# Kernel tuning notes

Hardware: AMD Instinct MI355X
Metric: run time of the kernel (lower is better)

The kernel has to match this reference:

```python
import jax, jax.numpy as jnp
import numpy as np

TAU = 10.0
AMP_FACTOR = 6.0
BLOCK = 10  # each pixel -> 8x8 value block padded by 1 -> 10x10


def _make_h(size=200, wavelength=5.32e-07, pixel_size=3.6e-05, distance=0.1):
    ll = pixel_size * size
    fi = 1.0 / ll
    wn = 2 * 3.1415926 / wavelength
    phi = np.fromfunction(
        lambda x, y: np.square((x - size // 2) * fi) + np.square((y - size // 2) * fi),
        shape=(size, size), dtype=np.float64)
    h = np.fft.fftshift(np.exp(1j * wn * distance) * np.exp(-1j * wavelength * np.pi * distance * phi))
    return h.astype(np.complex64)


def setup_inputs() -> dict:
    key = jax.random.key(0)
    B, S, P = 16, 200, 256
    ks = jax.random.split(key, 5)
    h = _make_h(size=S)
    return {
        "waves_real": jax.random.normal(ks[0], (B, S, S), jnp.float32),
        "waves_imag": jax.random.normal(ks[1], (B, S, S), jnp.float32),
        "h_real": jnp.asarray(h.real, jnp.float32),
        "h_imag": jnp.asarray(h.imag, jnp.float32),
        "voltage": jax.random.uniform(ks[2], (S, S, P), jnp.float32),
        "phase_func": jax.random.uniform(ks[3], (P,), jnp.float32),
        "intensity_func": jax.random.uniform(ks[4], (P,), jnp.float32),
    }


def _gumbel_softmax_hard(logits, key, tau):
    u = jax.random.uniform(key, logits.shape, logits.dtype, 1e-10, 1.0)
    g = -jnp.log(-jnp.log(u))
    y_soft = jax.nn.softmax((logits + g) / tau, axis=-1)
    y_hard = jax.nn.one_hot(jnp.argmax(y_soft, axis=-1), logits.shape[-1], dtype=logits.dtype)
    # straight-through estimator
    return y_hard + y_soft - jax.lax.stop_gradient(y_soft)


def reference(waves_real, waves_imag, h_real, h_imag, voltage, phase_func, intensity_func):
    waves = waves_real + 1j * waves_imag              # (B,S,S) complex
    h = h_real + 1j * h_imag                          # (S,S) complex transfer fn
    temp = jnp.fft.ifft2(jnp.fft.fft2(waves) * h)     # free-space diffraction

    k1, k2 = jax.random.split(jax.random.key(42))
    exp_j_phase = _gumbel_softmax_hard(voltage, k1, TAU) @ phase_func      # (S,S)
    amplitude = (_gumbel_softmax_hard(voltage, k2, TAU) @ intensity_func) * AMP_FACTOR
    phase_trig = amplitude * (jnp.cos(exp_j_phase) + 1j * jnp.sin(exp_j_phase))
    x = temp * phase_trig                             # (B,S,S) complex

    # pixel expansion: each pixel -> 10x10 block (value in center 8x8, zero border)
    B, S = x.shape[0], x.shape[1]
    pat = jnp.zeros((BLOCK, BLOCK), x.dtype).at[1:9, 1:9].set(1.0)
    out = (x[:, :, None, :, None] * pat[None, :, None, :][None]).reshape(B, S * BLOCK, S * BLOCK)
    return jnp.stack([out.real, out.imag], axis=-1)   # (B, 10S, 10S, 2) float
```

## Files before the change

kernel.cpp:

```cpp
#include <hip/hip_runtime.h>
#include <math.h>

constexpr int S = 200;
constexpr int NBATCH = 16;
constexpr int SS = S * S;
constexpr int FLAT = S * NBATCH;
constexpr int SLICE = S * FLAT;

struct TFOut { unsigned a, b; };

__host__ __device__ constexpr TFOut tf2x32(unsigned k0, unsigned k1,
                                           unsigned x0, unsigned x1) {
  unsigned ks2 = k0 ^ k1 ^ 0x1BD11BDAu;
  unsigned ks[3] = {k0, k1, ks2};
  const int R0[4] = {13, 15, 26, 6};
  const int R1[4] = {17, 29, 16, 24};
  x0 += ks[0]; x1 += ks[1];
  for (int i = 0; i < 5; ++i) {
    const int* R = (i & 1) ? R1 : R0;
    for (int j = 0; j < 4; ++j) {
      x0 += x1;
      x1 = (x1 << R[j]) | (x1 >> (32 - R[j]));
      x1 ^= x0;
    }
    x0 += ks[(i + 1) % 3];
    x1 += ks[(i + 2) % 3] + (unsigned)(i + 1);
  }
  return {x0, x1};
}

constexpr TFOut KEY1 = tf2x32(0u, 42u, 0u, 0u);
constexpr TFOut KEY2 = tf2x32(0u, 42u, 0u, 1u);

__device__ inline float bits_to_u(unsigned bits) {
  float f = __uint_as_float((bits >> 9) | 0x3f800000u) - 1.0f;
  f = f + 1e-10f;
  return fmaxf(1e-10f, f);
}

__device__ inline float u_to_g_exact(float u) {
  float l1 = (float)log((double)u);
  float l2 = (float)log((double)(-l1));
  return -l2;
}

__device__ inline float u_to_g_fast(float u) {
  float l1 = logf(u);
  float l2 = logf(-l1);
  return -l2;
}

__device__ inline unsigned ordf(float f) {
  unsigned u = __float_as_uint(f);
  return (u & 0x80000000u) ? ~u : (u | 0x80000000u);
}
__device__ inline float unordf(unsigned u) {
  return (u & 0x80000000u) ? __uint_as_float(u ^ 0x80000000u)
                           : __uint_as_float(~u);
}
__device__ inline unsigned long long packcand(float val, int p) {
  return ((unsigned long long)ordf(val) << 32) | (unsigned)(255 - p);
}
__device__ inline unsigned long long umax64(unsigned long long a,
                                            unsigned long long b) {
  return a > b ? a : b;
}
__device__ inline unsigned long long wave_max_ull(unsigned long long v) {
#pragma unroll
  for (int s = 32; s > 0; s >>= 1)
    v = umax64(v, (unsigned long long)__shfl_xor((unsigned long long)v, s, 64));
  return v;
}

__global__ __launch_bounds__(256) void gumbel_kernel(
    const float* __restrict__ voltage, const float* __restrict__ phase_func,
    const float* __restrict__ intensity_func, float2* __restrict__ PT) {
  const int q = blockIdx.x;
  const int p = threadIdx.x;
  const int wave = p >> 6, lane = p & 63;
  const unsigned idx = (unsigned)q * 256u + (unsigned)p;
  const float v = voltage[(size_t)q * 256 + p];
  TFOut r1 = tf2x32(KEY1.a, KEY1.b, 0u, idx);
  TFOut r2 = tf2x32(KEY2.a, KEY2.b, 0u, idx);
  const float u1 = bits_to_u(r1.a ^ r1.b);
  const float u2 = bits_to_u(r2.a ^ r2.b);
  const float c1a = (v + u_to_g_fast(u1)) * 0.1f;
  const float c2a = (v + u_to_g_fast(u2)) * 0.1f;

  __shared__ unsigned long long wred[2][4];
  __shared__ int wcnt[2][4];

  unsigned long long pk1 = wave_max_ull(packcand(c1a, p));
  unsigned long long pk2 = wave_max_ull(packcand(c2a, p));
  if (lane == 0) { wred[0][wave] = pk1; wred[1][wave] = pk2; }
  __syncthreads();
  unsigned long long b1 = umax64(umax64(wred[0][0], wred[0][1]),
                                 umax64(wred[0][2], wred[0][3]));
  unsigned long long b2 = umax64(umax64(wred[1][0], wred[1][1]),
                                 umax64(wred[1][2], wred[1][3]));
  const float eps = 1e-5f;
  const bool q1 = c1a >= unordf((unsigned)(b1 >> 32)) - eps;
  const bool q2 = c2a >= unordf((unsigned)(b2 >> 32)) - eps;
  unsigned long long bal1 = __ballot(q1);
  unsigned long long bal2 = __ballot(q2);
  if (lane == 0) { wcnt[0][wave] = __popcll(bal1); wcnt[1][wave] = __popcll(bal2); }
  __syncthreads();
  const int n1 = wcnt[0][0] + wcnt[0][1] + wcnt[0][2] + wcnt[0][3];
  const int n2 = wcnt[1][0] + wcnt[1][1] + wcnt[1][2] + wcnt[1][3];

  unsigned long long w1 = b1, w2 = b2;
  if (n1 > 1 || n2 > 1) {
    unsigned long long e1 = q1 ? packcand((v + u_to_g_exact(u1)) / 10.0f, p) : 0ull;
    unsigned long long e2 = q2 ? packcand((v + u_to_g_exact(u2)) / 10.0f, p) : 0ull;
    e1 = wave_max_ull(e1);
    e2 = wave_max_ull(e2);
    if (lane == 0) { wred[0][wave] = e1; wred[1][wave] = e2; }
    __syncthreads();
    w1 = umax64(umax64(wred[0][0], wred[0][1]), umax64(wred[0][2], wred[0][3]));
    w2 = umax64(umax64(wred[1][0], wred[1][1]), umax64(wred[1][2], wred[1][3]));
  }
  if (p == 0) {
    int i1 = 255 - (int)(w1 & 0xFFFFFFFFull);
    int i2 = 255 - (int)(w2 & 0xFFFFFFFFull);
    float phi = phase_func[i1];
    float amp = intensity_func[i2] * 6.0f;
    PT[q] = make_float2(amp * cosf(phi), amp * sinf(phi));
  }
}

__global__ __launch_bounds__(256) void build_tw(float2* __restrict__ tw) {
  int m = threadIdx.x;
  if (m < S) {
    double ang = -2.0 * 3.1415926535897932384626433832795 * (double)m / (double)S;
    tw[m] = make_float2((float)cos(ang), (float)sin(ang));
  }
}

__global__ __launch_bounds__(256) void build_tables(
    const float* __restrict__ h_real, const float* __restrict__ h_imag,
    const float2* __restrict__ tw, float2* __restrict__ F,
    float2* __restrict__ G, float2* __restrict__ Hc) {
  int idx = blockIdx.x * 256 + threadIdx.x;
  if (idx >= SS) return;
  int j = idx / S;
  int k = idx - j * S;
  int m = (j * k) % S;
  float2 t = tw[m];
  F[idx] = t;
  G[idx] = make_float2(t.x * 0.005f, -t.y * 0.005f);
  Hc[idx] = make_float2(h_real[idx], h_imag[idx]);
}

template <bool APERM, int MODE>
__global__ __launch_bounds__(256) void cgemm_ks(
    const float2* __restrict__ A, const float2* __restrict__ B,
    const float* __restrict__ Bre, const float* __restrict__ Bim,
    const float2* __restrict__ Hm, float2* __restrict__ Cp,
    int M, int N, int K, int KSlice) {
  __shared__ __align__(16) float2 As[16][64];
  __shared__ __align__(16) float2 Bs[16][64];
  const int tid = threadIdx.x;
  const int rowBase = blockIdx.x * 64;
  const int colBase = blockIdx.y * 64;
  const int Kbeg = blockIdx.z * KSlice;
  const int Kend = min(Kbeg + KSlice, K);

  const int a_m = tid >> 2;
  const int a_k4 = (tid & 3) * 4;
  const int b_k = tid >> 4;
  const int b_n4 = (tid & 15) * 4;
  const int tx4 = (tid & 15) * 4;
  const int ty4 = (tid >> 4) * 4;

  long arow;
  bool arow_ok;
  {
    int gm = rowBase + a_m;
    if (APERM) {
      int b = gm / S, i = gm - b * S;
      arow = (long)i * FLAT + (long)b * S;
      arow_ok = true;
    } else {
      arow_ok = (gm < M);
      arow = (long)gm * S;
    }
  }
  long bcol;
  int nmod = 0;
  bool bcol_ok;
  {
    int gn = colBase + b_n4;
    if (APERM) {
      bcol = gn;
      bcol_ok = (gn < N);
    } else {
      int b = gn / S;
      nmod = gn - b * S;
      bcol = (long)b * SS + nmod;
      bcol_ok = true;
    }
  }

  float2 acc[4][4];
#pragma unroll
  for (int i = 0; i < 4; ++i)
#pragma unroll
    for (int j = 0; j < 4; ++j) acc[i][j] = make_float2(0.f, 0.f);

  for (int k0 = Kbeg; k0 < Kend; k0 += 16) {
    const int gka = k0 + a_k4;
    float4 av0 = {0, 0, 0, 0}, av1 = {0, 0, 0, 0};
    if (arow_ok) {
      if (gka < Kend) av0 = *(const float4*)&A[arow + gka];
      if (gka + 2 < Kend) av1 = *(const float4*)&A[arow + gka + 2];
    }
    const int gkb = k0 + b_k;
    float4 bv0 = {0, 0, 0, 0}, bv1 = {0, 0, 0, 0};
    if (bcol_ok && gkb < Kend) {
      if (MODE == 2) {
        const long off = bcol + (long)gkb * S;
        float4 re4 = *(const float4*)&Bre[off];
        float4 im4 = *(const float4*)&Bim[off];
        bv0 = make_float4(re4.x, im4.x, re4.y, im4.y);
        bv1 = make_float4(re4.z, im4.z, re4.w, im4.w);
      } else {
        const float2* bp = &B[bcol + (long)gkb * S];
        bv0 = *(const float4*)bp;
        bv1 = *(const float4*)(bp + 2);
        if (MODE == 1) {
          const float2* hp = &Hm[(long)gkb * S + nmod];
          float4 h0 = *(const float4*)hp;
          float4 h1 = *(const float4*)(hp + 2);
          bv0 = make_float4(bv0.x * h0.x - bv0.y * h0.y, bv0.x * h0.y + bv0.y * h0.x,
                            bv0.z * h0.z - bv0.w * h0.w, bv0.z * h0.w + bv0.w * h0.z);
          bv1 = make_float4(bv1.x * h1.x - bv1.y * h1.y, bv1.x * h1.y + bv1.y * h1.x,
                            bv1.z * h1.z - bv1.w * h1.w, bv1.z * h1.w + bv1.w * h1.z);
        }
      }
    }
    __syncthreads();
    As[a_k4 + 0][a_m] = make_float2(av0.x, av0.y);
    As[a_k4 + 1][a_m] = make_float2(av0.z, av0.w);
    As[a_k4 + 2][a_m] = make_float2(av1.x, av1.y);
    As[a_k4 + 3][a_m] = make_float2(av1.z, av1.w);
    *(float4*)&Bs[b_k][b_n4] = bv0;
    *(float4*)&Bs[b_k][b_n4 + 2] = bv1;
    __syncthreads();
#pragma unroll
    for (int kk = 0; kk < 16; ++kk) {
      float4 aA = *(const float4*)&As[kk][ty4];
      float4 aB = *(const float4*)&As[kk][ty4 + 2];
      float4 bA = *(const float4*)&Bs[kk][tx4];
      float4 bB = *(const float4*)&Bs[kk][tx4 + 2];
      float2 a[4] = {{aA.x, aA.y}, {aA.z, aA.w}, {aB.x, aB.y}, {aB.z, aB.w}};
      float2 b[4] = {{bA.x, bA.y}, {bA.z, bA.w}, {bB.x, bB.y}, {bB.z, bB.w}};
#pragma unroll
      for (int i = 0; i < 4; ++i)
#pragma unroll
        for (int j = 0; j < 4; ++j) {
          acc[i][j].x = fmaf(a[i].x, b[j].x, fmaf(-a[i].y, b[j].y, acc[i][j].x));
          acc[i][j].y = fmaf(a[i].x, b[j].y, fmaf(a[i].y, b[j].x, acc[i][j].y));
        }
    }
  }
  float2* Co = Cp + (long)blockIdx.z * SLICE;
#pragma unroll
  for (int rr = 0; rr < 4; ++rr) {
    const int r = rowBase + ty4 + rr;
    const int cb = colBase + tx4;
    if (r < M && cb < N) {
      *(float4*)&Co[(long)r * N + cb] = make_float4(acc[rr][0].x, acc[rr][0].y,
                                                    acc[rr][1].x, acc[rr][1].y);
      *(float4*)&Co[(long)r * N + cb + 2] = make_float4(acc[rr][2].x, acc[rr][2].y,
                                                        acc[rr][3].x, acc[rr][3].y);
    }
  }
}

__global__ __launch_bounds__(256) void reduce4(
    const float4* __restrict__ P, float4* __restrict__ D) {
  int i = blockIdx.x * 256 + threadIdx.x;
  if (i >= SLICE / 2) return;
  float4 a = P[i], b = P[i + SLICE / 2], c = P[i + SLICE], d = P[i + 3 * SLICE / 2];
  D[i] = make_float4(a.x + b.x + c.x + d.x, a.y + b.y + c.y + d.y,
                     a.z + b.z + c.z + d.z, a.w + b.w + c.w + d.w);
}

__global__ __launch_bounds__(256) void reduce4_pt(
    const float2* __restrict__ P, const float2* __restrict__ PT,
    float2* __restrict__ D) {
  int i = blockIdx.x * 256 + threadIdx.x;
  if (i >= SLICE) return;
  float2 a = P[i], b = P[i + SLICE], c = P[i + 2 * SLICE], d = P[i + 3 * SLICE];
  float sx = a.x + b.x + c.x + d.x;
  float sy = a.y + b.y + c.y + d.y;
  float2 pt = PT[i % SS];
  D[i] = make_float2(sx * pt.x - sy * pt.y, sx * pt.y + sy * pt.x);
}

__global__ __launch_bounds__(256) void expand_kernel(
    const float2* __restrict__ Xc, float4* __restrict__ out) {
  unsigned q = blockIdx.x * 256u + threadIdx.x;
  unsigned p0 = q * 2u;
  unsigned b = p0 / 4000000u;
  unsigned rem = p0 - b * 4000000u;
  unsigned r = rem / 2000u;
  unsigned c0 = rem - r * 2000u;
  unsigned i = r / 10u;
  unsigned dr = r - i * 10u;
  float4 o = {0.f, 0.f, 0.f, 0.f};
  if (dr - 1u <= 7u) {
    unsigned j = c0 / 10u;
    unsigned dc = c0 - j * 10u;
    float2 xv = Xc[b * 40000u + i * 200u + j];
    if (dc != 0u) { o.x = xv.x; o.y = xv.y; }
    if (dc != 8u) { o.z = xv.x; o.w = xv.y; }
  }
  out[q] = o;
}

extern "C" void kernel_launch(void* const* d_in, const int* in_sizes, int n_in,
                              void* d_out, int out_size, void* d_ws, size_t ws_size,
                              hipStream_t stream) {
  const float* waves_real = (const float*)d_in[0];
  const float* waves_imag = (const float*)d_in[1];
  const float* h_real = (const float*)d_in[2];
  const float* h_imag = (const float*)d_in[3];
  const float* voltage = (const float*)d_in[4];
  const float* phase_func = (const float*)d_in[5];
  const float* intensity_func = (const float*)d_in[6];

  float2* TW   = (float2*)d_ws;
  float2* F    = TW + 256;
  float2* G    = F + SS;
  float2* Hc   = G + SS;
  float2* PT   = Hc + SS;
  float2* T1   = PT + SS;
  float2* T2   = T1 + SLICE;
  float2* T4   = T2 + SLICE;
  float2* Xc   = T4 + SLICE;
  float2* Part = Xc + SLICE;

  build_tw<<<1, 256, 0, stream>>>(TW);
  build_tables<<<157, 256, 0, stream>>>(h_real, h_imag, TW, F, G, Hc);
  gumbel_kernel<<<40000, 256, 0, stream>>>(voltage, phase_func, intensity_func, PT);

  dim3 gB(4, 50, 4);
  dim3 gA(50, 4, 4);

  cgemm_ks<false, 2><<<gB, 256, 0, stream>>>(F, nullptr, waves_real, waves_imag,
                                             nullptr, Part, S, FLAT, S, 50);
  reduce4<<<1250, 256, 0, stream>>>((const float4*)Part, (float4*)T1);
  cgemm_ks<true, 0><<<gA, 256, 0, stream>>>(T1, F, nullptr, nullptr, nullptr,
                                            Part, FLAT, S, S, 50);
  reduce4<<<1250, 256, 0, stream>>>((const float4*)Part, (float4*)T2);
  cgemm_ks<false, 1><<<gB, 256, 0, stream>>>(G, T2, nullptr, nullptr, Hc,
                                             Part, S, FLAT, S, 50);
  reduce4<<<1250, 256, 0, stream>>>((const float4*)Part, (float4*)T4);
  cgemm_ks<true, 0><<<gA, 256, 0, stream>>>(T4, G, nullptr, nullptr, nullptr,
                                            Part, FLAT, S, S, 50);
  reduce4_pt<<<2500, 256, 0, stream>>>(Part, PT, Xc);

  expand_kernel<<<125000, 256, 0, stream>>>(Xc, (float4*)d_out);
}
```

Baseline: 740.0 us.

## Replace FP32 split-K complex GEMMs with split-bf16 MFMA GEMMs and transposed layouts

Replaces the four FP32 CUDA-core complex DFT GEMMs and their split-K partial sums plus reduction kernels with an MFMA bf16 GEMM. Each operand is split into high and low bf16 parts, and three MFMAs per product approximate fp32 accuracy. Intermediates are stored transposed so each stage reads the previous one along K, and the final phase multiply is fused into the last GEMM epilogue. This removes the reduction passes and their partial-sum traffic. The costs are extra bf16 split work in the B loads, uncoalesced strided B loads in mode 0, and a precision risk from the bf16x3 approximation.

```diff
diff --git a/kernel.cpp b/kernel.cpp
--- a/kernel.cpp
+++ b/kernel.cpp
@@ -2,10 +2,15 @@
 #include <math.h>
 
 constexpr int S = 200;
-constexpr int NBATCH = 16;
 constexpr int SS = S * S;
-constexpr int FLAT = S * NBATCH;
-constexpr int SLICE = S * FLAT;
+constexpr int FLAT = 3200;
+constexpr int SLICE = 640000;
+constexpr int MP = 256;
+constexpr int KP = 224;
+constexpr int PS = MP * KP;
+
+typedef short short8 __attribute__((ext_vector_type(8)));
+typedef float float4v __attribute__((ext_vector_type(4)));
 
 struct TFOut { unsigned a, b; };
 
@@ -37,19 +42,16 @@
   f = f + 1e-10f;
   return fmaxf(1e-10f, f);
 }
-
 __device__ inline float u_to_g_exact(float u) {
   float l1 = (float)log((double)u);
   float l2 = (float)log((double)(-l1));
   return -l2;
 }
-
 __device__ inline float u_to_g_fast(float u) {
   float l1 = logf(u);
   float l2 = logf(-l1);
   return -l2;
 }
-
 __device__ inline unsigned ordf(float f) {
   unsigned u = __float_as_uint(f);
   return (u & 0x80000000u) ? ~u : (u | 0x80000000u);
@@ -136,170 +138,193 @@
   }
 }
 
-__global__ __launch_bounds__(256) void build_tables(
+__device__ inline unsigned short bf16_rne(float x) {
+  unsigned u = __float_as_uint(x);
+  return (unsigned short)((u + 0x7FFFu + ((u >> 16) & 1u)) >> 16);
+}
+__device__ inline void split_bf16(float x, unsigned short& h, unsigned short& l) {
+  h = bf16_rne(x);
+  float hf = __uint_as_float(((unsigned)h) << 16);
+  l = bf16_rne(x - hf);
+}
+
+__global__ __launch_bounds__(256) void build_planes(
+    const float2* __restrict__ tw, unsigned short* __restrict__ PL) {
+  int idx = blockIdx.x * 256 + threadIdx.x;
+  int m = idx / KP, k = idx - (idx / KP) * KP;
+  float fr = 0.f, fi = 0.f;
+  if (m < S && k < S) {
+    float2 t = tw[(m * k) % S];
+    fr = t.x; fi = t.y;
+  }
+  unsigned short h, l;
+  split_bf16(fr, h, l);          PL[0 * PS + idx] = h; PL[1 * PS + idx] = l;
+  split_bf16(fi, h, l);          PL[2 * PS + idx] = h; PL[3 * PS + idx] = l;
+  split_bf16(fr * 0.005f, h, l); PL[4 * PS + idx] = h; PL[5 * PS + idx] = l;
+  split_bf16(-fi * 0.005f, h, l);PL[6 * PS + idx] = h; PL[7 * PS + idx] = l;
+}
+
+__global__ __launch_bounds__(256) void build_ht(
     const float* __restrict__ h_real, const float* __restrict__ h_imag,
-    const float2* __restrict__ tw, float2* __restrict__ F,
-    float2* __restrict__ G, float2* __restrict__ Hc) {
+    float2* __restrict__ HT) {
   int idx = blockIdx.x * 256 + threadIdx.x;
   if (idx >= SS) return;
-  int j = idx / S;
-  int k = idx - j * S;
-  int m = (j * k) % S;
-  float2 t = tw[m];
-  F[idx] = t;
-  G[idx] = make_float2(t.x * 0.005f, -t.y * 0.005f);
-  Hc[idx] = make_float2(h_real[idx], h_imag[idx]);
-}
-
-template <bool APERM, int MODE>
-__global__ __launch_bounds__(256) void cgemm_ks(
-    const float2* __restrict__ A, const float2* __restrict__ B,
-    const float* __restrict__ Bre, const float* __restrict__ Bim,
-    const float2* __restrict__ Hm, float2* __restrict__ Cp,
-    int M, int N, int K, int KSlice) {
-  __shared__ __align__(16) float2 As[16][64];
-  __shared__ __align__(16) float2 Bs[16][64];
+  int k = idx / S, n = idx - (idx / S) * S;
+  HT[n * S + k] = make_float2(h_real[idx], h_imag[idx]);
+}
+
+template <int MODE, bool FINAL>
+__global__ __launch_bounds__(256) void gemm_mfma(
+    const unsigned short* __restrict__ APL, const float* __restrict__ Wre,
+    const float* __restrict__ Wim, const float2* __restrict__ Sprev,
+    const float2* __restrict__ HT, const float2* __restrict__ PT,
+    float2* __restrict__ Sout) {
+  __shared__ short As[4][64][40];
+  __shared__ short Bs[4][64][40];
   const int tid = threadIdx.x;
-  const int rowBase = blockIdx.x * 64;
-  const int colBase = blockIdx.y * 64;
-  const int Kbeg = blockIdx.z * KSlice;
-  const int Kend = min(Kbeg + KSlice, K);
-
-  const int a_m = tid >> 2;
-  const int a_k4 = (tid & 3) * 4;
-  const int b_k = tid >> 4;
-  const int b_n4 = (tid & 15) * 4;
-  const int tx4 = (tid & 15) * 4;
-  const int ty4 = (tid >> 4) * 4;
-
-  long arow;
-  bool arow_ok;
-  {
-    int gm = rowBase + a_m;
-    if (APERM) {
-      int b = gm / S, i = gm - b * S;
-      arow = (long)i * FLAT + (long)b * S;
-      arow_ok = true;
-    } else {
-      arow_ok = (gm < M);
-      arow = (long)gm * S;
-    }
-  }
-  long bcol;
-  int nmod = 0;
-  bool bcol_ok;
-  {
-    int gn = colBase + b_n4;
-    if (APERM) {
-      bcol = gn;
-      bcol_ok = (gn < N);
-    } else {
-      int b = gn / S;
-      nmod = gn - b * S;
-      bcol = (long)b * SS + nmod;
-      bcol_ok = true;
-    }
-  }
-
-  float2 acc[4][4];
-#pragma unroll
-  for (int i = 0; i < 4; ++i)
-#pragma unroll
-    for (int j = 0; j < 4; ++j) acc[i][j] = make_float2(0.f, 0.f);
-
-  for (int k0 = Kbeg; k0 < Kend; k0 += 16) {
-    const int gka = k0 + a_k4;
-    float4 av0 = {0, 0, 0, 0}, av1 = {0, 0, 0, 0};
-    if (arow_ok) {
-      if (gka < Kend) av0 = *(const float4*)&A[arow + gka];
-      if (gka + 2 < Kend) av1 = *(const float4*)&A[arow + gka + 2];
-    }
-    const int gkb = k0 + b_k;
-    float4 bv0 = {0, 0, 0, 0}, bv1 = {0, 0, 0, 0};
-    if (bcol_ok && gkb < Kend) {
-      if (MODE == 2) {
-        const long off = bcol + (long)gkb * S;
-        float4 re4 = *(const float4*)&Bre[off];
-        float4 im4 = *(const float4*)&Bim[off];
-        bv0 = make_float4(re4.x, im4.x, re4.y, im4.y);
-        bv1 = make_float4(re4.z, im4.z, re4.w, im4.w);
+  const int wave = tid >> 6, lane = tid & 63, quad = lane >> 4, l15 = lane & 15;
+  const int mb = blockIdx.x * 64;
+  const int cb = blockIdx.y * 64;
+
+  const int sp = tid >> 6;
+  const int sm = tid & 63;
+  const int sn = tid & 63;
+  const int sk0 = (tid >> 6) * 8;
+  const int cB = cb + sn;
+  const int bB = cB / S;
+  const int nB = cB - bB * S;
+
+  float4v accRR[2][2], accII[2][2], accRI[2][2], accIR[2][2];
+#pragma unroll
+  for (int i = 0; i < 2; ++i)
+#pragma unroll
+    for (int j = 0; j < 2; ++j) {
+      accRR[i][j] = (float4v){0.f, 0.f, 0.f, 0.f};
+      accII[i][j] = (float4v){0.f, 0.f, 0.f, 0.f};
+      accRI[i][j] = (float4v){0.f, 0.f, 0.f, 0.f};
+      accIR[i][j] = (float4v){0.f, 0.f, 0.f, 0.f};
+    }
+
+  for (int ch = 0; ch < 7; ++ch) {
+    const int kc = ch * 32;
+    const unsigned short* ap = APL + sp * PS + (mb + sm) * KP + kc;
+    short8 a0 = *(const short8*)(ap + 0);
+    short8 a1 = *(const short8*)(ap + 8);
+    short8 a2 = *(const short8*)(ap + 16);
+    short8 a3 = *(const short8*)(ap + 24);
+
+    unsigned short brh[8], brl[8], bih[8], bil[8];
+    const bool kok = (kc + sk0) < S;
+    float re[8], im[8];
+#pragma unroll
+    for (int j = 0; j < 8; ++j) { re[j] = 0.f; im[j] = 0.f; }
+    if (kok) {
+      if (MODE == 0) {
+#pragma unroll
+        for (int j = 0; j < 8; ++j) {
+          int k = kc + sk0 + j;
+          re[j] = Wre[(long)bB * SS + k * S + nB];
+          im[j] = Wim[(long)bB * SS + k * S + nB];
+        }
       } else {
-        const float2* bp = &B[bcol + (long)gkb * S];
-        bv0 = *(const float4*)bp;
-        bv1 = *(const float4*)(bp + 2);
-        if (MODE == 1) {
-          const float2* hp = &Hm[(long)gkb * S + nmod];
-          float4 h0 = *(const float4*)hp;
-          float4 h1 = *(const float4*)(hp + 2);
-          bv0 = make_float4(bv0.x * h0.x - bv0.y * h0.y, bv0.x * h0.y + bv0.y * h0.x,
-                            bv0.z * h0.z - bv0.w * h0.w, bv0.z * h0.w + bv0.w * h0.z);
-          bv1 = make_float4(bv1.x * h1.x - bv1.y * h1.y, bv1.x * h1.y + bv1.y * h1.x,
-                            bv1.z * h1.z - bv1.w * h1.w, bv1.z * h1.w + bv1.w * h1.z);
+        const float2* bp = &Sprev[(long)(bB * S + nB) * S + kc + sk0];
+#pragma unroll
+        for (int j = 0; j < 8; ++j) { re[j] = bp[j].x; im[j] = bp[j].y; }
+        if (MODE == 2) {
+          const float2* hp = &HT[(long)nB * S + kc + sk0];
+#pragma unroll
+          for (int j = 0; j < 8; ++j) {
+            float2 hv = hp[j];
+            float tr = re[j] * hv.x - im[j] * hv.y;
+            im[j] = re[j] * hv.y + im[j] * hv.x;
+            re[j] = tr;
+          }
         }
       }
     }
+#pragma unroll
+    for (int j = 0; j < 8; ++j) {
+      split_bf16(re[j], brh[j], brl[j]);
+      split_bf16(im[j], bih[j], bil[j]);
+    }
+
     __syncthreads();
-    As[a_k4 + 0][a_m] = make_float2(av0.x, av0.y);
-    As[a_k4 + 1][a_m] = make_float2(av0.z, av0.w);
-    As[a_k4 + 2][a_m] = make_float2(av1.x, av1.y);
-    As[a_k4 + 3][a_m] = make_float2(av1.z, av1.w);
-    *(float4*)&Bs[b_k][b_n4] = bv0;
-    *(float4*)&Bs[b_k][b_n4 + 2] = bv1;
+    *(short8*)&As[sp][sm][0] = a0;
+    *(short8*)&As[sp][sm][8] = a1;
+    *(short8*)&As[sp][sm][16] = a2;
+    *(short8*)&As[sp][sm][24] = a3;
+    short8 v0, v1, v2, v3;
+#pragma unroll
+    for (int j = 0; j < 8; ++j) {
+      v0[j] = (short)brh[j]; v1[j] = (short)brl[j];
+      v2[j] = (short)bih[j]; v3[j] = (short)bil[j];
+    }
+    *(short8*)&Bs[0][sn][sk0] = v0;
+    *(short8*)&Bs[1][sn][sk0] = v1;
+    *(short8*)&Bs[2][sn][sk0] = v2;
+    *(short8*)&Bs[3][sn][sk0] = v3;
     __syncthreads();
-#pragma unroll
-    for (int kk = 0; kk < 16; ++kk) {
-      float4 aA = *(const float4*)&As[kk][ty4];
-      float4 aB = *(const float4*)&As[kk][ty4 + 2];
-      float4 bA = *(const float4*)&Bs[kk][tx4];
-      float4 bB = *(const float4*)&Bs[kk][tx4 + 2];
-      float2 a[4] = {{aA.x, aA.y}, {aA.z, aA.w}, {aB.x, aB.y}, {aB.z, aB.w}};
-      float2 b[4] = {{bA.x, bA.y}, {bA.z, bA.w}, {bB.x, bB.y}, {bB.z, bB.w}};
-#pragma unroll
-      for (int i = 0; i < 4; ++i)
-#pragma unroll
-        for (int j = 0; j < 4; ++j) {
-          acc[i][j].x = fmaf(a[i].x, b[j].x, fmaf(-a[i].y, b[j].y, acc[i][j].x));
-          acc[i][j].y = fmaf(a[i].x, b[j].y, fmaf(a[i].y, b[j].x, acc[i][j].y));
+
+    short8 Arh[2], Arl[2], Aih[2], Ail[2], Brh[2], Brl[2], Bih[2], Bil[2];
+#pragma unroll
+    for (int t = 0; t < 2; ++t) {
+      int mr = (wave & 1) * 32 + t * 16 + l15;
+      Arh[t] = *(const short8*)&As[0][mr][quad * 8];
+      Arl[t] = *(const short8*)&As[1][mr][quad * 8];
+      Aih[t] = *(const short8*)&As[2][mr][quad * 8];
+      Ail[t] = *(const short8*)&As[3][mr][quad * 8];
+      int nr = (wave >> 1) * 32 + t * 16 + l15;
+      Brh[t] = *(const short8*)&Bs[0][nr][quad * 8];
+      Brl[t] = *(const short8*)&Bs[1][nr][quad * 8];
+      Bih[t] = *(const short8*)&Bs[2][nr][quad * 8];
+      Bil[t] = *(const short8*)&Bs[3][nr][quad * 8];
+    }
+#pragma unroll
+    for (int mi = 0; mi < 2; ++mi)
+#pragma unroll
+      for (int ni = 0; ni < 2; ++ni) {
+        accRR[mi][ni] = __builtin_amdgcn_mfma_f32_16x16x32_bf16(Arh[mi], Brh[ni], accRR[mi][ni], 0, 0, 0);
+        accRR[mi][ni] = __builtin_amdgcn_mfma_f32_16x16x32_bf16(Arh[mi], Brl[ni], accRR[mi][ni], 0, 0, 0);
+        accRR[mi][ni] = __builtin_amdgcn_mfma_f32_16x16x32_bf16(Arl[mi], Brh[ni], accRR[mi][ni], 0, 0, 0);
+        accII[mi][ni] = __builtin_amdgcn_mfma_f32_16x16x32_bf16(Aih[mi], Bih[ni], accII[mi][ni], 0, 0, 0);
+        accII[mi][ni] = __builtin_amdgcn_mfma_f32_16x16x32_bf16(Aih[mi], Bil[ni], accII[mi][ni], 0, 0, 0);
+        accII[mi][ni] = __builtin_amdgcn_mfma_f32_16x16x32_bf16(Ail[mi], Bih[ni], accII[mi][ni], 0, 0, 0);
+        accRI[mi][ni] = __builtin_amdgcn_mfma_f32_16x16x32_bf16(Arh[mi], Bih[ni], accRI[mi][ni], 0, 0, 0);
+        accRI[mi][ni] = __builtin_amdgcn_mfma_f32_16x16x32_bf16(Arh[mi], Bil[ni], accRI[mi][ni], 0, 0, 0);
+        accRI[mi][ni] = __builtin_amdgcn_mfma_f32_16x16x32_bf16(Arl[mi], Bih[ni], accRI[mi][ni], 0, 0, 0);
+        accIR[mi][ni] = __builtin_amdgcn_mfma_f32_16x16x32_bf16(Aih[mi], Brh[ni], accIR[mi][ni], 0, 0, 0);
+        accIR[mi][ni] = __builtin_amdgcn_mfma_f32_16x16x32_bf16(Aih[mi], Brl[ni], accIR[mi][ni], 0, 0, 0);
+        accIR[mi][ni] = __builtin_amdgcn_mfma_f32_16x16x32_bf16(Ail[mi], Brh[ni], accIR[mi][ni], 0, 0, 0);
+      }
+  }
+
+#pragma unroll
+  for (int mi = 0; mi < 2; ++mi)
+#pragma unroll
+    for (int ni = 0; ni < 2; ++ni) {
+      int cg = cb + (wave >> 1) * 32 + ni * 16 + l15;
+      int b = cg / S;
+      int n = cg - b * S;
+#pragma unroll
+      for (int r = 0; r < 4; ++r) {
+        int m = mb + (wave & 1) * 32 + mi * 16 + quad * 4 + r;
+        if (m < S) {
+          float Cr = accRR[mi][ni][r] - accII[mi][ni][r];
+          float Ci = accRI[mi][ni][r] + accIR[mi][ni][r];
+          if (FINAL) {
+            float2 pt = PT[n * S + m];
+            float tr = Cr * pt.x - Ci * pt.y;
+            Ci = Cr * pt.y + Ci * pt.x;
+            Cr = tr;
+          }
+          Sout[(long)(b * S + m) * S + n] = make_float2(Cr, Ci);
         }
-    }
-  }
-  float2* Co = Cp + (long)blockIdx.z * SLICE;
-#pragma unroll
-  for (int rr = 0; rr < 4; ++rr) {
-    const int r = rowBase + ty4 + rr;
-    const int cb = colBase + tx4;
-    if (r < M && cb < N) {
-      *(float4*)&Co[(long)r * N + cb] = make_float4(acc[rr][0].x, acc[rr][0].y,
-                                                    acc[rr][1].x, acc[rr][1].y);
-      *(float4*)&Co[(long)r * N + cb + 2] = make_float4(acc[rr][2].x, acc[rr][2].y,
-                                                        acc[rr][3].x, acc[rr][3].y);
-    }
-  }
-}
-
-__global__ __launch_bounds__(256) void reduce4(
-    const float4* __restrict__ P, float4* __restrict__ D) {
-  int i = blockIdx.x * 256 + threadIdx.x;
-  if (i >= SLICE / 2) return;
-  float4 a = P[i], b = P[i + SLICE / 2], c = P[i + SLICE], d = P[i + 3 * SLICE / 2];
-  D[i] = make_float4(a.x + b.x + c.x + d.x, a.y + b.y + c.y + d.y,
-                     a.z + b.z + c.z + d.z, a.w + b.w + c.w + d.w);
-}
-
-__global__ __launch_bounds__(256) void reduce4_pt(
-    const float2* __restrict__ P, const float2* __restrict__ PT,
-    float2* __restrict__ D) {
-  int i = blockIdx.x * 256 + threadIdx.x;
-  if (i >= SLICE) return;
-  float2 a = P[i], b = P[i + SLICE], c = P[i + 2 * SLICE], d = P[i + 3 * SLICE];
-  float sx = a.x + b.x + c.x + d.x;
-  float sy = a.y + b.y + c.y + d.y;
-  float2 pt = PT[i % SS];
-  D[i] = make_float2(sx * pt.x - sy * pt.y, sx * pt.y + sy * pt.x);
+      }
+    }
 }
 
 __global__ __launch_bounds__(256) void expand_kernel(
-    const float2* __restrict__ Xc, float4* __restrict__ out) {
+    const float2* __restrict__ S4, float4* __restrict__ out) {
   unsigned q = blockIdx.x * 256u + threadIdx.x;
   unsigned p0 = q * 2u;
   unsigned b = p0 / 4000000u;
@@ -312,7 +337,7 @@
   if (dr - 1u <= 7u) {
     unsigned j = c0 / 10u;
     unsigned dc = c0 - j * 10u;
-    float2 xv = Xc[b * 40000u + i * 200u + j];
+    float2 xv = S4[(b * 200u + j) * 200u + i];
     if (dc != 0u) { o.x = xv.x; o.y = xv.y; }
     if (dc != 8u) { o.z = xv.x; o.w = xv.y; }
   }
@@ -330,36 +355,31 @@
   const float* phase_func = (const float*)d_in[5];
   const float* intensity_func = (const float*)d_in[6];
 
-  float2* TW   = (float2*)d_ws;
-  float2* F    = TW + 256;
-  float2* G    = F + SS;
-  float2* Hc   = G + SS;
-  float2* PT   = Hc + SS;
-  float2* T1   = PT + SS;
-  float2* T2   = T1 + SLICE;
-  float2* T4   = T2 + SLICE;
-  float2* Xc   = T4 + SLICE;
-  float2* Part = Xc + SLICE;
+  float2* TW = (float2*)d_ws;
+  float2* HT = TW + 256;
+  float2* PT = HT + SS;
+  float2* S1 = PT + SS;
+  float2* S2 = S1 + SLICE;
+  float2* S3 = S2 + SLICE;
+  float2* S4 = S3 + SLICE;
+  unsigned short* PL = (unsigned short*)(S4 + SLICE);
 
   build_tw<<<1, 256, 0, stream>>>(TW);
-  build_tables<<<157, 256, 0, stream>>>(h_real, h_imag, TW, F, G, Hc);
+  build_planes<<<224, 256, 0, stream>>>(TW, PL);
+  build_ht<<<157, 256, 0, stream>>>(h_real, h_imag, HT);
   gumbel_kernel<<<40000, 256, 0, stream>>>(voltage, phase_func, intensity_func, PT);
 
-  dim3 gB(4, 50, 4);
-  dim3 gA(50, 4, 4);
-
-  cgemm_ks<false, 2><<<gB, 256, 0, stream>>>(F, nullptr, waves_real, waves_imag,
-                                             nullptr, Part, S, FLAT, S, 50);
-  reduce4<<<1250, 256, 0, stream>>>((const float4*)Part, (float4*)T1);
-  cgemm_ks<true, 0><<<gA, 256, 0, stream>>>(T1, F, nullptr, nullptr, nullptr,
-                                            Part, FLAT, S, S, 50);
-  reduce4<<<1250, 256, 0, stream>>>((const float4*)Part, (float4*)T2);
-  cgemm_ks<false, 1><<<gB, 256, 0, stream>>>(G, T2, nullptr, nullptr, Hc,
-                                             Part, S, FLAT, S, 50);
-  reduce4<<<1250, 256, 0, stream>>>((const float4*)Part, (float4*)T4);
-  cgemm_ks<true, 0><<<gA, 256, 0, stream>>>(T4, G, nullptr, nullptr, nullptr,
-                                            Part, FLAT, S, S, 50);
-  reduce4_pt<<<2500, 256, 0, stream>>>(Part, PT, Xc);
-
-  expand_kernel<<<125000, 256, 0, stream>>>(Xc, (float4*)d_out);
-}
+  const unsigned short* FP = PL;
+  const unsigned short* GP = PL + 4 * PS;
+  dim3 g(4, 50);
+  gemm_mfma<0, false><<<g, 256, 0, stream>>>(FP, waves_real, waves_imag,
+                                             nullptr, nullptr, nullptr, S1);
+  gemm_mfma<1, false><<<g, 256, 0, stream>>>(FP, nullptr, nullptr, S1,
+                                             nullptr, nullptr, S2);
+  gemm_mfma<2, false><<<g, 256, 0, stream>>>(GP, nullptr, nullptr, S2,
+                                             HT, nullptr, S3);
+  gemm_mfma<1, true><<<g, 256, 0, stream>>>(GP, nullptr, nullptr, S3,
+                                            nullptr, PT, S4);
+
+  expand_kernel<<<125000, 256, 0, stream>>>(S4, (float4*)d_out);
+}
```

Measured after the change: 681.8 us. 7.9% less time.
